# Performance work log

Hardware: AMD Instinct MI355X
Metric: run time of the kernel (lower is better)

## Reference

```python
import jax, jax.numpy as jnp
import numpy as np

B, N, DIM = 4, 2048, 512
H, HD = 8, 64  # n_heads, head_dim; inner_dim = H*HD = 512
SCALE = 1.0 / float(np.sqrt(HD))

def setup_inputs() -> dict:
    key = jax.random.key(0)
    k1, k2, k3 = jax.random.split(key, 3)
    x = jax.random.normal(k1, (B, N, DIM), dtype=jnp.float32)
    w_qkv = jax.random.normal(k2, (DIM, 3 * H * HD), dtype=jnp.float32) * 0.02
    w_out = jax.random.normal(k3, (H * HD, DIM), dtype=jnp.float32) * 0.02
    b_out = jnp.zeros((DIM,), dtype=jnp.float32)
    return {"x": x, "w_qkv": w_qkv, "w_out": w_out, "b_out": b_out}

def reference(x, w_qkv, w_out, b_out):
    b, n, c = x.shape
    qkv = x @ w_qkv                                   # [B,N,3*H*HD]
    qkv = qkv.reshape(b, n, 3, H, HD)
    q = qkv[:, :, 0].transpose(0, 2, 1, 3)            # [B,H,N,HD]
    k = qkv[:, :, 1].transpose(0, 2, 1, 3)
    v = qkv[:, :, 2].transpose(0, 2, 1, 3)
    # non-softmax attention: (Q K^T) V scaled by 1/sqrt(d) and 1/N
    attn = jnp.einsum('bhnd,bhmd->bhnm', q, k) * (SCALE / n)  # [B,H,N,N]
    out = jnp.einsum('bhnm,bhmd->bhnd', attn, v)               # [B,H,N,HD]
    out = out.transpose(0, 2, 1, 3).reshape(b, n, H * HD)
    return out @ w_out + b_out
```

## Files before the change

### kernel.cpp

```cpp
#include <hip/hip_runtime.h>
#include <stdint.h>

typedef unsigned short u16;
typedef __attribute__((ext_vector_type(8))) __bf16 bf16x8;
typedef __attribute__((ext_vector_type(8))) unsigned short u16x8;
typedef __attribute__((ext_vector_type(4))) float f32x4;

#define AS1 __attribute__((address_space(1)))
#define AS3 __attribute__((address_space(3)))

__device__ __forceinline__ u16 f2bf(float f) {
  uint32_t u = __builtin_bit_cast(uint32_t, f);
  u += 0x7FFFu + ((u >> 16) & 1u);
  return (u16)(u >> 16);
}
__device__ __forceinline__ float bf2f(u16 h) {
  uint32_t u = ((uint32_t)h) << 16;
  return __builtin_bit_cast(float, u);
}
__device__ __forceinline__ void gload16(const void* g, void* l) {
  __builtin_amdgcn_global_load_lds((AS1 void*)g, (AS3 void*)l, 16, 0, 0);
}

__global__ __launch_bounds__(256) void prep(const float4* __restrict__ x,
                                            ushort4* __restrict__ x_bf,
                                            const float* __restrict__ w,
                                            u16* __restrict__ wt) {
  __shared__ u16 tile[32][33];
  const int bid = blockIdx.x;
  if (bid < 4096) {
    int i = bid * 256 + threadIdx.x;
    float4 v = x[i];
    ushort4 o;
    o.x = f2bf(v.x); o.y = f2bf(v.y); o.z = f2bf(v.z); o.w = f2bf(v.w);
    x_bf[i] = o;
  } else {
    int tb = bid - 4096;
    int c0 = (tb % 48) * 32, r0 = (tb / 48) * 32;
    int tx = threadIdx.x & 31, ty = threadIdx.x >> 5;
    #pragma unroll
    for (int rr = ty; rr < 32; rr += 8)
      tile[rr][tx] = f2bf(w[(size_t)(r0 + rr) * 1536 + c0 + tx]);
    __syncthreads();
    #pragma unroll
    for (int rr = ty; rr < 32; rr += 8)
      wt[(size_t)(c0 + rr) * 512 + r0 + tx] = tile[tx][rr];
  }
}

template<bool OUT_F32, bool BIAS, int NFRAG>
__global__ __launch_bounds__(256) void gemm_bt64(
    const u16* __restrict__ A, int lda, long long strideA,
    const u16* __restrict__ Bt, int ldb, long long strideB,
    void* __restrict__ C, int ldc, long long strideC,
    const float* __restrict__ bias, int K)
{
  constexpr int BN = NFRAG * 32;
  const int nwgx = gridDim.x, nwgy = gridDim.y;
  const int nwg = nwgx * nwgy * gridDim.z;
  const int hw = blockIdx.x + nwgx * (blockIdx.y + nwgy * blockIdx.z);
  const int cpx = nwg >> 3;
  const int swz = (hw & 7) * cpx + (hw >> 3);
  const int bx = swz % nwgx;
  const int tmp = swz / nwgx;
  const int by = tmp % nwgy;
  const int bz = tmp / nwgy;

  const int bcol = bx * BN;
  const int brow = by * 128;
  const u16* Ab = A + (size_t)bz * strideA;
  const u16* Bb = Bt + (size_t)bz * strideB;

  __shared__ u16 Asm[128 * 64];
  __shared__ u16 Bsm[BN * 64];

  const int tid = threadIdx.x;
  const int wid = tid >> 6;
  const int lane = tid & 63;
  const int fr = lane & 15, fq = lane >> 4;
  const int wr = wid >> 1, wc = wid & 1;
  const int srow = lane >> 3;
  const int scol = ((lane & 7) ^ srow) * 8;
  const int xr = (fr & 7) * 8;

  f32x4 acc[4][NFRAG];
  #pragma unroll
  for (int m = 0; m < 4; ++m)
    #pragma unroll
    for (int n = 0; n < NFRAG; ++n)
      acc[m][n] = (f32x4)0.0f;

  for (int kt = 0; kt < K; kt += 64) {
    #pragma unroll
    for (int q = 0; q < 4; ++q) {
      int seg = wid * 4 + q;
      int row = seg * 8 + srow;
      gload16(Ab + (size_t)(brow + row) * lda + kt + scol, &Asm[seg * 512]);
    }
    #pragma unroll
    for (int q = 0; q < NFRAG; ++q) {
      int seg = wid * NFRAG + q;
      int row = seg * 8 + srow;
      gload16(Bb + (size_t)(bcol + row) * ldb + kt + scol, &Bsm[seg * 512]);
    }
    __syncthreads();

    #pragma unroll
    for (int kk = 0; kk < 2; ++kk) {
      bf16x8 af[4], bg[NFRAG];
      #pragma unroll
      for (int m = 0; m < 4; ++m)
        af[m] = *(const bf16x8*)&Asm[(wr * 64 + m * 16 + fr) * 64 + ((kk * 32 + fq * 8) ^ xr)];
      #pragma unroll
      for (int n = 0; n < NFRAG; ++n)
        bg[n] = *(const bf16x8*)&Bsm[(wc * (NFRAG * 16) + n * 16 + fr) * 64 + ((kk * 32 + fq * 8) ^ xr)];
      #pragma unroll
      for (int m = 0; m < 4; ++m)
        #pragma unroll
        for (int n = 0; n < NFRAG; ++n)
          acc[m][n] = __builtin_amdgcn_mfma_f32_16x16x32_bf16(af[m], bg[n], acc[m][n], 0, 0, 0);
    }
    __syncthreads();
  }

  #pragma unroll
  for (int m = 0; m < 4; ++m) {
    #pragma unroll
    for (int n = 0; n < NFRAG; ++n) {
      #pragma unroll
      for (int j = 0; j < 4; ++j) {
        int row = brow + wr * 64 + m * 16 + fq * 4 + j;
        int col = bcol + wc * (NFRAG * 16) + n * 16 + fr;
        float v = acc[m][n][j];
        if constexpr (OUT_F32) {
          if constexpr (BIAS) v += bias[col];
          ((float*)C)[(size_t)bz * strideC + (size_t)row * ldc + col] = v;
        } else {
          ((u16*)C)[(size_t)bz * strideC + (size_t)row * ldc + col] = f2bf(v);
        }
      }
    }
  }
}

#define KTV_SPLIT 16
__global__ __launch_bounds__(256) void ktv_partial(const u16* __restrict__ qkv,
                                                   float* __restrict__ Mpart) {
  const int s = blockIdx.x;
  const int bh = blockIdx.y;
  const int b = bh >> 3, h = bh & 7;
  const int t = threadIdx.x;
  __shared__ alignas(16) u16 SM[2 * 64 * 136];
  u16* Kt = SM;
  u16* Vt = SM + 64 * 136;
  float* Msm = (float*)SM;

  const u16* base = qkv + (size_t)b * 2048 * 1536 + (size_t)(s * 128) * 1536;
  u16x8 v[8];
  #pragma unroll
  for (int it = 0; it < 8; ++it) {
    int c = it * 256 + t;
    int n = c >> 4, part = c & 15;
    int col = (part < 8) ? (512 + h * 64 + part * 8) : (1024 + h * 64 + (part - 8) * 8);
    v[it] = *(const u16x8*)(base + (size_t)n * 1536 + col);
  }
  #pragma unroll
  for (int it = 0; it < 8; ++it) {
    int c = it * 256 + t;
    int n = c >> 4, part = c & 15;
    int p8 = part & 7;
    u16* mat = (part < 8) ? Kt : Vt;
    int ncol = n ^ (p8 << 3);
    #pragma unroll
    for (int j = 0; j < 8; ++j)
      mat[(p8 * 8 + j) * 136 + ncol] = v[it][j];
  }
  __syncthreads();

  const int wid = t >> 6, lane = t & 63;
  const int fr = lane & 15, fq = lane >> 4;
  const int kbase = wid * 32 + fq * 8;
  f32x4 acc[4][4];
  #pragma unroll
  for (int m = 0; m < 4; ++m)
    #pragma unroll
    for (int n = 0; n < 4; ++n) acc[m][n] = (f32x4)0.0f;
  bf16x8 af[4], bg[4];
  #pragma unroll
  for (int m = 0; m < 4; ++m) {
    int d = m * 16 + fr;
    af[m] = *(const bf16x8*)&Kt[d * 136 + (kbase ^ ((d >> 3) << 3))];
  }
  #pragma unroll
  for (int n = 0; n < 4; ++n) {
    int e = n * 16 + fr;
    bg[n] = *(const bf16x8*)&Vt[e * 136 + (kbase ^ ((e >> 3) << 3))];
  }
  #pragma unroll
  for (int m = 0; m < 4; ++m)
    #pragma unroll
    for (int n = 0; n < 4; ++n)
      acc[m][n] = __builtin_amdgcn_mfma_f32_16x16x32_bf16(af[m], bg[n], acc[m][n], 0, 0, 0);
  __syncthreads();

  #pragma unroll
  for (int p = 0; p < 4; ++p) {
    if (wid == p) {
      #pragma unroll
      for (int m = 0; m < 4; ++m)
        #pragma unroll
        for (int n = 0; n < 4; ++n)
          #pragma unroll
          for (int j = 0; j < 4; ++j) {
            float* q = &Msm[(m * 16 + fq * 4 + j) * 64 + n * 16 + fr];
            *q = (p == 0) ? acc[m][n][j] : (*q + acc[m][n][j]);
          }
    }
    __syncthreads();
  }
  float4* d4 = (float4*)(Mpart + ((size_t)bh * KTV_SPLIT + s) * 4096);
  const float4* s4 = (const float4*)Msm;
  #pragma unroll
  for (int r = 0; r < 4; ++r) d4[t + r * 256] = s4[t + r * 256];
}

__global__ __launch_bounds__(256) void reduce_m(const float* __restrict__ Mpart,
                                                float* __restrict__ M, float scale) {
  int i = blockIdx.x * 256 + threadIdx.x;
  int bh = i >> 12;
  int off = i & 4095;
  const float* src = Mpart + ((size_t)bh * KTV_SPLIT) * 4096 + off;
  float s = 0.f;
  #pragma unroll
  for (int p = 0; p < KTV_SPLIT; ++p) s += src[(size_t)p * 4096];
  M[i] = s * scale;
}

__global__ __launch_bounds__(256) void make_pt2(const float* __restrict__ M,
                                                const float* __restrict__ w_out,
                                                u16* __restrict__ Pt) {
  const int ct = blockIdx.x;
  const int bh = blockIdx.y;
  const int b = bh >> 3, h = bh & 7;
  const int t = threadIdx.x;
  __shared__ float Msm[64 * 64];
  {
    const float4* src = (const float4*)(M + (size_t)bh * 4096);
    float4* dst = (float4*)Msm;
    #pragma unroll
    for (int r = 0; r < 4; ++r) dst[t + r * 256] = src[t + r * 256];
  }
  __syncthreads();
  const int c = ct * 64 + (t & 63);
  const int d0 = (t >> 6) * 16;
  float acc[16];
  #pragma unroll
  for (int j = 0; j < 16; ++j) acc[j] = 0.f;
  const float* wcol = w_out + (size_t)h * 64 * 512 + c;
  #pragma unroll 4
  for (int e = 0; e < 64; ++e) {
    float w = wcol[(size_t)e * 512];
    #pragma unroll
    for (int j = 0; j < 16; ++j)
      acc[j] += Msm[(d0 + j) * 64 + e] * w;
  }
  ushort4 ov[4];
  #pragma unroll
  for (int r = 0; r < 4; ++r) {
    ov[r].x = f2bf(acc[r * 4 + 0]);
    ov[r].y = f2bf(acc[r * 4 + 1]);
    ov[r].z = f2bf(acc[r * 4 + 2]);
    ov[r].w = f2bf(acc[r * 4 + 3]);
  }
  ushort4* dst = (ushort4*)(Pt + (size_t)b * 262144 + (size_t)c * 512 + h * 64 + d0);
  #pragma unroll
  for (int r = 0; r < 4; ++r) dst[r] = ov[r];
}

extern "C" void kernel_launch(void* const* d_in, const int* in_sizes, int n_in,
                              void* d_out, int out_size, void* d_ws, size_t ws_size,
                              hipStream_t stream) {
  const float* x     = (const float*)d_in[0];
  const float* w_qkv = (const float*)d_in[1];
  const float* w_out = (const float*)d_in[2];
  const float* b_out = (const float*)d_in[3];
  float* out = (float*)d_out;
  char* ws = (char*)d_ws;
  const long long MB = 1ll << 20;

  u16*   x_bf   = (u16*)(ws);
  u16*   wqkv_t = (u16*)(ws + 8 * MB);
  u16*   qkv    = (u16*)(ws + 10 * MB);
  float* Mpart  = (float*)(ws + 34 * MB);
  float* M      = (float*)(ws);
  u16*   Pt     = (u16*)(ws + 42 * MB);

  prep<<<dim3(4096 + 768), dim3(256), 0, stream>>>(
      (const float4*)x, (ushort4*)x_bf, w_qkv, wqkv_t);
  gemm_bt64<false, false, 4><<<dim3(12, 64, 1), dim3(256), 0, stream>>>(
      x_bf, 512, 0ll, wqkv_t, 512, 0ll, qkv, 1536, 0ll, nullptr, 512);
  ktv_partial<<<dim3(KTV_SPLIT, 32), dim3(256), 0, stream>>>(qkv, Mpart);
  reduce_m<<<dim3(512), dim3(256), 0, stream>>>(Mpart, M, 0.125f / 2048.0f);
  make_pt2<<<dim3(8, 32), dim3(256), 0, stream>>>(M, w_out, Pt);
  gemm_bt64<true, true, 2><<<dim3(8, 16, 4), dim3(256), 0, stream>>>(
      qkv, 1536, 2048ll * 1536, Pt, 512, 262144ll, out, 512, 2048ll * 512, b_out, 512);
}
```

Measured before the change: 61.50 us.

## Double-buffer GEMM LDS tiles and fold partial-sum reduction into Pt kernel

The bf16 GEMM kernel now keeps two LDS buffers and issues the global-to-LDS loads for the next K tile before computing on the current one, so memory latency can overlap with MFMA work and one barrier per iteration is removed. The separate reduce_m kernel is dropped, and make_pt3 sums the KTV_SPLIT partial M blocks and applies the scale while filling its shared tile. This saves one launch and one global round trip for M. In exchange LDS use per block doubles, which may lower occupancy, and each make_pt3 block (8 per bh) redundantly re-reduces the same partials.

```diff
diff --git a/kernel.cpp b/kernel.cpp
--- a/kernel.cpp
+++ b/kernel.cpp
@@ -49,7 +49,7 @@
 }
 
 template<bool OUT_F32, bool BIAS, int NFRAG>
-__global__ __launch_bounds__(256) void gemm_bt64(
+__global__ __launch_bounds__(256) void gemm_db(
     const u16* __restrict__ A, int lda, long long strideA,
     const u16* __restrict__ Bt, int ldb, long long strideB,
     void* __restrict__ C, int ldc, long long strideC,
@@ -71,8 +71,8 @@
   const u16* Ab = A + (size_t)bz * strideA;
   const u16* Bb = Bt + (size_t)bz * strideB;
 
-  __shared__ u16 Asm[128 * 64];
-  __shared__ u16 Bsm[BN * 64];
+  __shared__ u16 Asm[2][128 * 64];
+  __shared__ u16 Bsm[2][BN * 64];
 
   const int tid = threadIdx.x;
   const int wid = tid >> 6;
@@ -90,30 +90,35 @@
     for (int n = 0; n < NFRAG; ++n)
       acc[m][n] = (f32x4)0.0f;
 
-  for (int kt = 0; kt < K; kt += 64) {
+  auto stage = [&](int buf, int kt) {
     #pragma unroll
     for (int q = 0; q < 4; ++q) {
       int seg = wid * 4 + q;
       int row = seg * 8 + srow;
-      gload16(Ab + (size_t)(brow + row) * lda + kt + scol, &Asm[seg * 512]);
+      gload16(Ab + (size_t)(brow + row) * lda + kt + scol, &Asm[buf][seg * 512]);
     }
     #pragma unroll
     for (int q = 0; q < NFRAG; ++q) {
       int seg = wid * NFRAG + q;
       int row = seg * 8 + srow;
-      gload16(Bb + (size_t)(bcol + row) * ldb + kt + scol, &Bsm[seg * 512]);
-    }
-    __syncthreads();
-
+      gload16(Bb + (size_t)(bcol + row) * ldb + kt + scol, &Bsm[buf][seg * 512]);
+    }
+  };
+
+  stage(0, 0);
+  __syncthreads();
+  int cur = 0;
+  for (int kt = 0; kt < K; kt += 64) {
+    if (kt + 64 < K) stage(cur ^ 1, kt + 64);
     #pragma unroll
     for (int kk = 0; kk < 2; ++kk) {
       bf16x8 af[4], bg[NFRAG];
       #pragma unroll
       for (int m = 0; m < 4; ++m)
-        af[m] = *(const bf16x8*)&Asm[(wr * 64 + m * 16 + fr) * 64 + ((kk * 32 + fq * 8) ^ xr)];
+        af[m] = *(const bf16x8*)&Asm[cur][(wr * 64 + m * 16 + fr) * 64 + ((kk * 32 + fq * 8) ^ xr)];
       #pragma unroll
       for (int n = 0; n < NFRAG; ++n)
-        bg[n] = *(const bf16x8*)&Bsm[(wc * (NFRAG * 16) + n * 16 + fr) * 64 + ((kk * 32 + fq * 8) ^ xr)];
+        bg[n] = *(const bf16x8*)&Bsm[cur][(wc * (NFRAG * 16) + n * 16 + fr) * 64 + ((kk * 32 + fq * 8) ^ xr)];
       #pragma unroll
       for (int m = 0; m < 4; ++m)
         #pragma unroll
@@ -121,6 +126,7 @@
           acc[m][n] = __builtin_amdgcn_mfma_f32_16x16x32_bf16(af[m], bg[n], acc[m][n], 0, 0, 0);
     }
     __syncthreads();
+    cur ^= 1;
   }
 
   #pragma unroll
@@ -224,31 +230,29 @@
   for (int r = 0; r < 4; ++r) d4[t + r * 256] = s4[t + r * 256];
 }
 
-__global__ __launch_bounds__(256) void reduce_m(const float* __restrict__ Mpart,
-                                                float* __restrict__ M, float scale) {
-  int i = blockIdx.x * 256 + threadIdx.x;
-  int bh = i >> 12;
-  int off = i & 4095;
-  const float* src = Mpart + ((size_t)bh * KTV_SPLIT) * 4096 + off;
-  float s = 0.f;
-  #pragma unroll
-  for (int p = 0; p < KTV_SPLIT; ++p) s += src[(size_t)p * 4096];
-  M[i] = s * scale;
-}
-
-__global__ __launch_bounds__(256) void make_pt2(const float* __restrict__ M,
+__global__ __launch_bounds__(256) void make_pt3(const float* __restrict__ Mpart,
                                                 const float* __restrict__ w_out,
-                                                u16* __restrict__ Pt) {
+                                                u16* __restrict__ Pt, float scale) {
   const int ct = blockIdx.x;
   const int bh = blockIdx.y;
   const int b = bh >> 3, h = bh & 7;
   const int t = threadIdx.x;
   __shared__ float Msm[64 * 64];
   {
-    const float4* src = (const float4*)(M + (size_t)bh * 4096);
+    const float4* src = (const float4*)(Mpart + (size_t)bh * KTV_SPLIT * 4096);
     float4* dst = (float4*)Msm;
     #pragma unroll
-    for (int r = 0; r < 4; ++r) dst[t + r * 256] = src[t + r * 256];
+    for (int r = 0; r < 4; ++r) {
+      int f4 = t + r * 256;
+      float4 s; s.x = 0.f; s.y = 0.f; s.z = 0.f; s.w = 0.f;
+      #pragma unroll 4
+      for (int p = 0; p < KTV_SPLIT; ++p) {
+        float4 g = src[p * 1024 + f4];
+        s.x += g.x; s.y += g.y; s.z += g.z; s.w += g.w;
+      }
+      s.x *= scale; s.y *= scale; s.z *= scale; s.w *= scale;
+      dst[f4] = s;
+    }
   }
   __syncthreads();
   const int c = ct * 64 + (t & 63);
@@ -292,16 +296,14 @@
   u16*   wqkv_t = (u16*)(ws + 8 * MB);
   u16*   qkv    = (u16*)(ws + 10 * MB);
   float* Mpart  = (float*)(ws + 34 * MB);
-  float* M      = (float*)(ws);
   u16*   Pt     = (u16*)(ws + 42 * MB);
 
   prep<<<dim3(4096 + 768), dim3(256), 0, stream>>>(
       (const float4*)x, (ushort4*)x_bf, w_qkv, wqkv_t);
-  gemm_bt64<false, false, 4><<<dim3(12, 64, 1), dim3(256), 0, stream>>>(
+  gemm_db<false, false, 4><<<dim3(12, 64, 1), dim3(256), 0, stream>>>(
       x_bf, 512, 0ll, wqkv_t, 512, 0ll, qkv, 1536, 0ll, nullptr, 512);
   ktv_partial<<<dim3(KTV_SPLIT, 32), dim3(256), 0, stream>>>(qkv, Mpart);
-  reduce_m<<<dim3(512), dim3(256), 0, stream>>>(Mpart, M, 0.125f / 2048.0f);
-  make_pt2<<<dim3(8, 32), dim3(256), 0, stream>>>(M, w_out, Pt);
-  gemm_bt64<true, true, 2><<<dim3(8, 16, 4), dim3(256), 0, stream>>>(
+  make_pt3<<<dim3(8, 32), dim3(256), 0, stream>>>(Mpart, w_out, Pt, 0.125f / 2048.0f);
+  gemm_db<true, true, 2><<<dim3(8, 16, 4), dim3(256), 0, stream>>>(
       qkv, 1536, 2048ll * 1536, Pt, 512, 262144ll, out, 512, 2048ll * 512, b_out, 512);
 }
```

New measurement: 70.62 us. +14.8%, slower.
